# Performance work log

Measured on AMD Instinct MI355X. Metric: run time of the kernel, lower is better.

The kernel has to match this reference:

```python
import jax, jax.numpy as jnp
import numpy as np

NUM_HEADS = 16

def _rms_norm(x):
    # F.rms_norm over last dim, eps = dtype machine epsilon (torch default eps=None)
    eps = jnp.finfo(jnp.float32).eps
    ms = jnp.mean(jnp.square(x.astype(jnp.float32)), axis=-1, keepdims=True)
    return (x.astype(jnp.float32) * jax.lax.rsqrt(ms + eps)).astype(x.dtype)

def _rotary_tables(T, head_dim):
    # inv_freq = (1/1024)**linspace(0,1,head_dim//4), padded with zeros to head_dim//2
    quarter = head_dim // 4
    inv_freq = (1.0 / 1024.0) ** jnp.linspace(0.0, 1.0, quarter, dtype=jnp.float32)
    inv_freq = jnp.concatenate([inv_freq, jnp.zeros(quarter, dtype=jnp.float32)])
    t = jnp.arange(T, dtype=jnp.float32)
    theta = t[:, None] * inv_freq[None, :]          # [T, head_dim//2]
    return jnp.cos(theta), jnp.sin(theta)

def _rotary(x, cos, sin):
    # x: [B, T, H, hd]; rotate in fp32, cast back
    xf = x.astype(jnp.float32)
    x1, x2 = jnp.split(xf, 2, axis=-1)
    c = cos[None, :, None, :]
    s = sin[None, :, None, :]
    y1 = x1 * c + x2 * s
    y2 = -x1 * s + x2 * c
    return jnp.concatenate([y1, y2], axis=-1).astype(x.dtype)

def setup_inputs() -> dict:
    key = jax.random.key(0)
    ks = jax.random.split(key, 7)
    B, T, D = 1, 2048, 1024
    sc = 1.0 / np.sqrt(D)
    return {
        "x": jax.random.normal(ks[0], (B, T, D), jnp.float32),
        "vi": jax.random.normal(ks[1], (B, T, D), jnp.float32),
        "Wq": jax.random.normal(ks[2], (D, D), jnp.float32) * sc,
        "Wk": jax.random.normal(ks[3], (D, D), jnp.float32) * sc,
        "Wv": jax.random.normal(ks[4], (D, D), jnp.float32) * sc,
        "Wproj": jax.random.normal(ks[5], (D, D), jnp.float32) * sc,
        "lambdas": jnp.array([0.5, 0.5], jnp.float32),
    }

def reference(x, vi, Wq, Wk, Wv, Wproj, lambdas):
    B, T, D = x.shape
    H = NUM_HEADS
    hd = D // H
    q = (x @ Wq.T).reshape(B, T, H, hd)
    k = (x @ Wk.T).reshape(B, T, H, hd)
    v = (x @ Wv.T).reshape(B, T, H, hd)
    # value residual: lambda-mixed v
    v = lambdas[0] * v + lambdas[1] * vi.reshape(B, T, H, hd)
    q, k = _rms_norm(q), _rms_norm(k)
    cos, sin = _rotary_tables(T, hd)
    q, k = _rotary(q, cos, sin), _rotary(k, cos, sin)
    # causal attention, default flex_attention scale = 1/sqrt(head_dim)
    scores = jnp.einsum('bthd,bshd->bhts', q, k) / jnp.sqrt(jnp.float32(hd))
    causal = jnp.tril(jnp.ones((T, T), dtype=bool))
    scores = jnp.where(causal[None, None], scores, jnp.float32(-1e30))
    attn = jax.nn.softmax(scores, axis=-1)
    y = jnp.einsum('bhts,bshd->bthd', attn, v).reshape(B, T, D)
    return y @ Wproj.T
```

## Files before the change

### kernel.cpp

```cpp
#include <hip/hip_runtime.h>
#include <math.h>

#define T_SEQ 2048
#define D_MODEL 1024
#define NH 16
#define HD 64

typedef unsigned short ushort_t;
typedef unsigned int uint_t;
typedef short short8 __attribute__((ext_vector_type(8)));
typedef float floatx4 __attribute__((ext_vector_type(4)));

__device__ __forceinline__ ushort_t f2bf(float f) {
    uint_t u = __float_as_uint(f);
    u += 0x7FFFu + ((u >> 16) & 1u);
    return (ushort_t)(u >> 16);
}
__device__ __forceinline__ uint_t pack2(float a, float b) {
    return (uint_t)f2bf(a) | ((uint_t)f2bf(b) << 16);
}
__device__ __forceinline__ void cp16(ushort_t* dst, const ushort_t* src) {
    uint4 a = ((const uint4*)src)[0];
    uint4 b = ((const uint4*)src)[1];
    ((uint4*)dst)[0] = a;
    ((uint4*)dst)[1] = b;
}
__device__ __forceinline__ void gload16(const ushort_t* g, ushort_t* l) {
    __builtin_amdgcn_global_load_lds(
        (const __attribute__((address_space(1))) void*)g,
        (__attribute__((address_space(3))) void*)l, 16, 0, 0);
}

#define LDK 72

__global__ __launch_bounds__(256) void to_bf16(
        const float* __restrict__ x,  const float* __restrict__ wq,
        const float* __restrict__ wk, const float* __restrict__ wv,
        const float* __restrict__ wp,
        ushort_t* __restrict__ xb,  ushort_t* __restrict__ wqb,
        ushort_t* __restrict__ wkb, ushort_t* __restrict__ wvb,
        ushort_t* __restrict__ wpb)
{
    size_t i = (size_t)blockIdx.x * 256 + threadIdx.x;
    const float* src; ushort_t* dst; size_t off;
    if (i < 262144)      { src = x;  dst = xb;  off = i; }
    else if (i < 393216) { src = wq; dst = wqb; off = i - 262144; }
    else if (i < 524288) { src = wk; dst = wkb; off = i - 393216; }
    else if (i < 655360) { src = wv; dst = wvb; off = i - 524288; }
    else                 { src = wp; dst = wpb; off = i - 655360; }
    float4 f0 = ((const float4*)src)[off * 2];
    float4 f1 = ((const float4*)src)[off * 2 + 1];
    uint4 u;
    u.x = pack2(f0.x, f0.y); u.y = pack2(f0.z, f0.w);
    u.z = pack2(f1.x, f1.y); u.w = pack2(f1.z, f1.w);
    ((uint4*)dst)[off] = u;
}

__global__ __launch_bounds__(256) void gemm_qkv(
        const ushort_t* __restrict__ xb,
        const ushort_t* __restrict__ Wqb, const ushort_t* __restrict__ Wkb,
        const ushort_t* __restrict__ Wvb,
        const float* __restrict__ vi, const float* __restrict__ lam,
        ushort_t* __restrict__ qb, ushort_t* __restrict__ kb,
        ushort_t* __restrict__ vbt)
{
    const int z = blockIdx.z;
    const ushort_t* __restrict__ W = (z == 0) ? Wqb : (z == 1) ? Wkb : Wvb;
    const int row0 = blockIdx.y * 64;
    const int col0 = blockIdx.x * 128;

    __shared__ ushort_t As[2 * 64 * 64];
    __shared__ ushort_t Bs[2 * 128 * 64];

    const int tid = threadIdx.x;
    const int wave = tid >> 6, lane = tid & 63;
    const int wm = wave >> 1, wn = wave & 1;
    const int l15 = lane & 15, quad = lane >> 4;
    const int srow  = tid >> 3;
    const int sslot = (tid & 7) ^ (srow & 7);

    floatx4 acc[2][4];
    #pragma unroll
    for (int i = 0; i < 2; ++i)
        #pragma unroll
        for (int j = 0; j < 4; ++j)
            acc[i][j] = (floatx4){0.f, 0.f, 0.f, 0.f};

    auto stageAB = [&](int k0, int p) {
        ushort_t* Ap = As + p * 4096;
        ushort_t* Bp = Bs + p * 8192;
        #pragma unroll
        for (int c = 0; c < 2; ++c)
            gload16(xb + (size_t)(row0 + c * 32 + srow) * D_MODEL + k0 + sslot * 8,
                    Ap + c * 2048 + tid * 8);
        #pragma unroll
        for (int c = 0; c < 4; ++c)
            gload16(W + (size_t)(col0 + c * 32 + srow) * D_MODEL + k0 + sslot * 8,
                    Bp + c * 2048 + tid * 8);
    };

    stageAB(0, 0);
    int cur = 0;
    for (int knext = 64; knext <= D_MODEL; knext += 64) {
        const bool haveNext = (knext < D_MODEL);
        if (haveNext) {
            stageAB(knext, cur ^ 1);
            asm volatile("s_waitcnt vmcnt(6)" ::: "memory");
        } else {
            asm volatile("s_waitcnt vmcnt(0)" ::: "memory");
        }
        __builtin_amdgcn_s_barrier();
        const ushort_t* Ac = As + cur * 4096;
        const ushort_t* Bc = Bs + cur * 8192;
        #pragma unroll
        for (int kh = 0; kh < 2; ++kh) {
            const int slot = ((kh * 4 + quad) ^ (l15 & 7)) << 3;
            short8 a[2], b[4];
            #pragma unroll
            for (int i = 0; i < 2; ++i)
                a[i] = *(const short8*)(Ac + (32 * wm + i * 16 + l15) * 64 + slot);
            #pragma unroll
            for (int j = 0; j < 4; ++j)
                b[j] = *(const short8*)(Bc + (64 * wn + j * 16 + l15) * 64 + slot);
            #pragma unroll
            for (int i = 0; i < 2; ++i)
                #pragma unroll
                for (int j = 0; j < 4; ++j)
                    acc[i][j] = __builtin_amdgcn_mfma_f32_16x16x32_bf16(a[i], b[j], acc[i][j], 0, 0, 0);
        }
        asm volatile("" ::: "memory");
        __builtin_amdgcn_s_barrier();
        cur ^= 1;
    }

    if (z < 2) {
        ushort_t* __restrict__ o = (z == 0) ? qb : kb;
        const float oscale = (z == 0) ? 0.125f : 1.0f;
        const int hbase = col0 + 64 * wn;
        const float eps = 1.1920929e-7f;
        const float fr = exp2f(-10.0f * (float)l15 / 15.0f);
        #pragma unroll
        for (int i = 0; i < 2; ++i)
            #pragma unroll
            for (int r = 0; r < 4; ++r) {
                const int t = row0 + 32 * wm + i * 16 + quad * 4 + r;
                float v0 = acc[i][0][r], v1 = acc[i][1][r];
                float v2 = acc[i][2][r], v3 = acc[i][3][r];
                float ss = v0 * v0 + v1 * v1 + v2 * v2 + v3 * v3;
                ss += __shfl_xor(ss, 1);
                ss += __shfl_xor(ss, 2);
                ss += __shfl_xor(ss, 4);
                ss += __shfl_xor(ss, 8);
                const float sc = rsqrtf(ss * (1.0f / 64.0f) + eps);
                v0 *= sc; v1 *= sc; v2 *= sc; v3 *= sc;
                const float th = (float)t * fr;
                const float cs = cosf(th), sn = sinf(th);
                const float y0 = v0 * cs + v2 * sn;
                const float y2 = v2 * cs - v0 * sn;
                const size_t rb = (size_t)t * D_MODEL + hbase;
                o[rb +  0 + l15] = f2bf(y0 * oscale);
                o[rb + 16 + l15] = f2bf(v1 * oscale);
                o[rb + 32 + l15] = f2bf(y2 * oscale);
                o[rb + 48 + l15] = f2bf(v3 * oscale);
            }
    } else {
        const float l0 = lam[0], l1 = lam[1];
        #pragma unroll
        for (int i = 0; i < 2; ++i)
            #pragma unroll
            for (int j = 0; j < 4; ++j) {
                const int tb = row0 + 32 * wm + i * 16 + quad * 4;
                const int jj = col0 + 64 * wn + j * 16 + l15;
                float b0 = l0 * acc[i][j][0] + l1 * vi[(size_t)(tb + 0) * D_MODEL + jj];
                float b1 = l0 * acc[i][j][1] + l1 * vi[(size_t)(tb + 1) * D_MODEL + jj];
                float b2 = l0 * acc[i][j][2] + l1 * vi[(size_t)(tb + 2) * D_MODEL + jj];
                float b3 = l0 * acc[i][j][3] + l1 * vi[(size_t)(tb + 3) * D_MODEL + jj];
                uint2 u;
                u.x = pack2(b0, b1);
                u.y = pack2(b2, b3);
                *(uint2*)(vbt + (size_t)jj * T_SEQ + tb) = u;
            }
    }
}

__global__ __launch_bounds__(256) void attn(
        const ushort_t* __restrict__ qb, const ushort_t* __restrict__ kb,
        const ushort_t* __restrict__ vbt, ushort_t* __restrict__ yb,
        float* __restrict__ Opart, float* __restrict__ Lpart)
{
    const int h = blockIdx.y;
    const int x = blockIdx.x;
    int qt, ct_begin, ct_end, pidx;
    if (x < 16) {
        qt = 31 - x;
        const int mid = (qt + 2) >> 1;
        ct_begin = 0; ct_end = mid;
        pidx = ((h * 16 + (qt - 16)) << 1);
    } else if (x < 32) {
        qt = 47 - x;
        const int mid = (qt + 2) >> 1;
        ct_begin = mid; ct_end = qt + 1;
        pidx = ((h * 16 + (qt - 16)) << 1) + 1;
    } else {
        qt = 47 - x;
        ct_begin = 0; ct_end = qt + 1;
        pidx = -1;
    }
    const int t0 = qt * 64;

    __shared__ ushort_t Ks[2 * 64 * 64];
    __shared__ ushort_t Vs[2 * 64 * 64];
    __shared__ ushort_t QPs[64 * LDK];

    const int tid = threadIdx.x;
    const int wave = tid >> 6, lane = tid & 63;
    const int l15 = lane & 15, quad = lane >> 4;
    const int r4 = tid >> 2, c4 = (tid & 3) * 16;
    const int srow  = tid >> 3;
    const int sslot = (tid & 7) ^ (srow & 7);
    const int bx = l15 & 7;

    cp16(QPs + r4 * LDK + c4, qb + (size_t)(t0 + r4) * D_MODEL + h * HD + c4);
    __syncthreads();
    short8 qf[2];
    qf[0] = *(const short8*)(QPs + (16 * wave + l15) * LDK + 0  + quad * 8);
    qf[1] = *(const short8*)(QPs + (16 * wave + l15) * LDK + 32 + quad * 8);

    auto stageKV = [&](int kt, int p) {
        const int s0 = kt * 64;
        ushort_t* Kp = Ks + p * 4096;
        ushort_t* Vp = Vs + p * 4096;
        gload16(kb  + (size_t)(s0 + srow)      * D_MODEL + h * HD + sslot * 8, Kp + tid * 8);
        gload16(kb  + (size_t)(s0 + 32 + srow) * D_MODEL + h * HD + sslot * 8, Kp + 2048 + tid * 8);
        gload16(vbt + (size_t)(h * HD + srow)      * T_SEQ + s0 + sslot * 8,   Vp + tid * 8);
        gload16(vbt + (size_t)(h * HD + 32 + srow) * T_SEQ + s0 + sslot * 8,   Vp + 2048 + tid * 8);
    };

    float l_acc[4];
    floatx4 O[4];
    #pragma unroll
    for (int r = 0; r < 4; ++r) l_acc[r] = 0.0f;
    #pragma unroll
    for (int d = 0; d < 4; ++d) O[d] = (floatx4){0.f, 0.f, 0.f, 0.f};

    stageKV(ct_begin, 0);
    int cur = 0;
    for (int kt = ct_begin; kt < ct_end; ++kt) {
        const bool haveNext = (kt + 1 < ct_end);
        if (haveNext) {
            stageKV(kt + 1, cur ^ 1);
            asm volatile("s_waitcnt vmcnt(4)" ::: "memory");
        } else {
            asm volatile("s_waitcnt vmcnt(0)" ::: "memory");
        }
        __builtin_amdgcn_s_barrier();

        const ushort_t* Kc = Ks + cur * 4096;
        const ushort_t* Vc = Vs + cur * 4096;

        floatx4 sa[4];
        #pragma unroll
        for (int ct = 0; ct < 4; ++ct) {
            const ushort_t* krow = Kc + (ct * 16 + l15) * 64;
            short8 b0 = *(const short8*)(krow + ((quad ^ bx) << 3));
            short8 b1 = *(const short8*)(krow + (((quad + 4) ^ bx) << 3));
            floatx4 t4 = (floatx4){0.f, 0.f, 0.f, 0.f};
            t4 = __builtin_amdgcn_mfma_f32_16x16x32_bf16(qf[0], b0, t4, 0, 0, 0);
            t4 = __builtin_amdgcn_mfma_f32_16x16x32_bf16(qf[1], b1, t4, 0, 0, 0);
            sa[ct] = t4;
        }
        if (kt == qt) {
            #pragma unroll
            for (int ct = 0; ct < 4; ++ct)
                #pragma unroll
                for (int r = 0; r < 4; ++r) {
                    int trow = 16 * wave + quad * 4 + r;
                    int scol = ct * 16 + l15;
                    if (scol > trow) sa[ct][r] = -1e30f;
                }
        }
        float p[4][4];
        #pragma unroll
        for (int ct = 0; ct < 4; ++ct)
            #pragma unroll
            for (int r = 0; r < 4; ++r) {
                p[ct][r] = __expf(sa[ct][r] - 8.0f);
                l_acc[r] += p[ct][r];
            }

        #pragma unroll
        for (int ct = 0; ct < 4; ++ct)
            #pragma unroll
            for (int r = 0; r < 4; ++r)
                QPs[(16 * wave + quad * 4 + r) * LDK + ct * 16 + l15] = f2bf(p[ct][r]);

        short8 pa0 = *(const short8*)(QPs + (16 * wave + l15) * LDK + 0  + quad * 8);
        short8 pa1 = *(const short8*)(QPs + (16 * wave + l15) * LDK + 32 + quad * 8);
        #pragma unroll
        for (int dt = 0; dt < 4; ++dt) {
            const ushort_t* vrow = Vc + (dt * 16 + l15) * 64;
            short8 vb0 = *(const short8*)(vrow + ((quad ^ bx) << 3));
            short8 vb1 = *(const short8*)(vrow + (((quad + 4) ^ bx) << 3));
            O[dt] = __builtin_amdgcn_mfma_f32_16x16x32_bf16(pa0, vb0, O[dt], 0, 0, 0);
            O[dt] = __builtin_amdgcn_mfma_f32_16x16x32_bf16(pa1, vb1, O[dt], 0, 0, 0);
        }

        asm volatile("" ::: "memory");
        __builtin_amdgcn_s_barrier();
        cur ^= 1;
    }

    float l_run[4];
    #pragma unroll
    for (int r = 0; r < 4; ++r) {
        float s = l_acc[r];
        s += __shfl_xor(s, 1);
        s += __shfl_xor(s, 2);
        s += __shfl_xor(s, 4);
        s += __shfl_xor(s, 8);
        l_run[r] = s;
    }

    if (pidx < 0) {
        #pragma unroll
        for (int r = 0; r < 4; ++r) {
            const float inv_l = 1.0f / l_run[r];
            const int t = t0 + 16 * wave + quad * 4 + r;
            #pragma unroll
            for (int dt = 0; dt < 4; ++dt)
                yb[(size_t)t * D_MODEL + h * HD + dt * 16 + l15] = f2bf(O[dt][r] * inv_l);
        }
    } else {
        float* __restrict__ Op = Opart + (size_t)pidx * 4096;
        #pragma unroll
        for (int r = 0; r < 4; ++r) {
            const int row = 16 * wave + quad * 4 + r;
            #pragma unroll
            for (int dt = 0; dt < 4; ++dt)
                Op[row * 64 + dt * 16 + l15] = O[dt][r];
            if (l15 == 0) Lpart[(size_t)pidx * 64 + row] = l_run[r];
        }
    }
}

__global__ __launch_bounds__(256) void attn_combine(
        const float* __restrict__ Opart, const float* __restrict__ Lpart,
        ushort_t* __restrict__ yb)
{
    const int qtp = blockIdx.x;
    const int h   = blockIdx.y;
    const int tid = threadIdx.x;
    const int row  = tid >> 2;
    const int dseg = (tid & 3) * 16;
    const int p0 = (h * 16 + qtp) * 2;

    const float l0 = Lpart[(size_t)p0 * 64 + row];
    const float l1 = Lpart[((size_t)p0 + 1) * 64 + row];
    const float inv = 1.0f / (l0 + l1);

    const float* O0 = Opart + (size_t)p0 * 4096 + row * 64 + dseg;
    const float* O1 = O0 + 4096;

    uint_t u[8];
    #pragma unroll
    for (int g = 0; g < 4; ++g) {
        float4 a = ((const float4*)O0)[g];
        float4 b = ((const float4*)O1)[g];
        u[g * 2 + 0] = pack2((a.x + b.x) * inv, (a.y + b.y) * inv);
        u[g * 2 + 1] = pack2((a.z + b.z) * inv, (a.w + b.w) * inv);
    }
    const int t = (16 + qtp) * 64 + row;
    uint4* dst = (uint4*)(yb + (size_t)t * D_MODEL + h * HD + dseg);
    dst[0] = make_uint4(u[0], u[1], u[2], u[3]);
    dst[1] = make_uint4(u[4], u[5], u[6], u[7]);
}

__global__ __launch_bounds__(256) void gemm_proj(
        const ushort_t* __restrict__ yb, const ushort_t* __restrict__ Wpb,
        float* __restrict__ out)
{
    const int row0 = blockIdx.y * 64;
    const int col0 = blockIdx.x * 128;

    __shared__ ushort_t As[2 * 64 * 64];
    __shared__ ushort_t Bs[2 * 128 * 64];

    const int tid = threadIdx.x;
    const int wave = tid >> 6, lane = tid & 63;
    const int wm = wave >> 1, wn = wave & 1;
    const int l15 = lane & 15, quad = lane >> 4;
    const int srow  = tid >> 3;
    const int sslot = (tid & 7) ^ (srow & 7);

    floatx4 acc[2][4];
    #pragma unroll
    for (int i = 0; i < 2; ++i)
        #pragma unroll
        for (int j = 0; j < 4; ++j)
            acc[i][j] = (floatx4){0.f, 0.f, 0.f, 0.f};

    auto stageAB = [&](int k0, int p) {
        ushort_t* Ap = As + p * 4096;
        ushort_t* Bp = Bs + p * 8192;
        #pragma unroll
        for (int c = 0; c < 2; ++c)
            gload16(yb + (size_t)(row0 + c * 32 + srow) * D_MODEL + k0 + sslot * 8,
                    Ap + c * 2048 + tid * 8);
        #pragma unroll
        for (int c = 0; c < 4; ++c)
            gload16(Wpb + (size_t)(col0 + c * 32 + srow) * D_MODEL + k0 + sslot * 8,
                    Bp + c * 2048 + tid * 8);
    };

    stageAB(0, 0);
    int cur = 0;
    for (int knext = 64; knext <= D_MODEL; knext += 64) {
        const bool haveNext = (knext < D_MODEL);
        if (haveNext) {
            stageAB(knext, cur ^ 1);
            asm volatile("s_waitcnt vmcnt(6)" ::: "memory");
        } else {
            asm volatile("s_waitcnt vmcnt(0)" ::: "memory");
        }
        __builtin_amdgcn_s_barrier();
        const ushort_t* Ac = As + cur * 4096;
        const ushort_t* Bc = Bs + cur * 8192;
        #pragma unroll
        for (int kh = 0; kh < 2; ++kh) {
            const int slot = ((kh * 4 + quad) ^ (l15 & 7)) << 3;
            short8 a[2], b[4];
            #pragma unroll
            for (int i = 0; i < 2; ++i)
                a[i] = *(const short8*)(Ac + (32 * wm + i * 16 + l15) * 64 + slot);
            #pragma unroll
            for (int j = 0; j < 4; ++j)
                b[j] = *(const short8*)(Bc + (64 * wn + j * 16 + l15) * 64 + slot);
            #pragma unroll
            for (int i = 0; i < 2; ++i)
                #pragma unroll
                for (int j = 0; j < 4; ++j)
                    acc[i][j] = __builtin_amdgcn_mfma_f32_16x16x32_bf16(a[i], b[j], acc[i][j], 0, 0, 0);
        }
        asm volatile("" ::: "memory");
        __builtin_amdgcn_s_barrier();
        cur ^= 1;
    }

    #pragma unroll
    for (int i = 0; i < 2; ++i)
        #pragma unroll
        for (int j = 0; j < 4; ++j) {
            const int t = row0 + 32 * wm + i * 16 + quad * 4;
            const int jj = col0 + 64 * wn + j * 16 + l15;
            #pragma unroll
            for (int r = 0; r < 4; ++r)
                out[(size_t)(t + r) * D_MODEL + jj] = acc[i][j][r];
        }
}

extern "C" void kernel_launch(void* const* d_in, const int* in_sizes, int n_in,
                              void* d_out, int out_size, void* d_ws, size_t ws_size,
                              hipStream_t stream) {
    (void)in_sizes; (void)n_in; (void)out_size; (void)ws_size;
    const float* x   = (const float*)d_in[0];
    const float* vi  = (const float*)d_in[1];
    const float* Wq  = (const float*)d_in[2];
    const float* Wk  = (const float*)d_in[3];
    const float* Wv  = (const float*)d_in[4];
    const float* Wp  = (const float*)d_in[5];
    const float* lam = (const float*)d_in[6];

    char* base = (char*)d_ws;
    ushort_t* xb  = (ushort_t*)(base);
    ushort_t* wqb = (ushort_t*)(base + (size_t)4  * 1048576);
    ushort_t* wkb = (ushort_t*)(base + (size_t)6  * 1048576);
    ushort_t* wvb = (ushort_t*)(base + (size_t)8  * 1048576);
    ushort_t* wpb = (ushort_t*)(base + (size_t)10 * 1048576);
    ushort_t* qb  = (ushort_t*)(base + (size_t)12 * 1048576);
    ushort_t* kb  = (ushort_t*)(base + (size_t)16 * 1048576);
    ushort_t* vbt = (ushort_t*)(base + (size_t)20 * 1048576);
    ushort_t* yb  = (ushort_t*)(base + (size_t)24 * 1048576);
    float* Opart  = (float*)(base);
    float* Lpart  = (float*)(base + (size_t)8 * 1048576);
    float* out = (float*)d_out;

    to_bf16<<<dim3(786432 / 256), 256, 0, stream>>>(x, Wq, Wk, Wv, Wp, xb, wqb, wkb, wvb, wpb);
    gemm_qkv<<<dim3(8, 32, 3), 256, 0, stream>>>(xb, wqb, wkb, wvb, vi, lam, qb, kb, vbt);
    attn<<<dim3(48, 16), 256, 0, stream>>>(qb, kb, vbt, yb, Opart, Lpart);
    attn_combine<<<dim3(16, 16), 256, 0, stream>>>(Opart, Lpart, yb);
    gemm_proj<<<dim3(8, 32), 256, 0, stream>>>(yb, wpb, out);
}
```

Measured before the change: 149.7 us.

## Enlarge GEMM tiles to 128 rows and rebalance attention split-K across query tiles

Both projection GEMMs now use 128x128 output tiles per block with 4x4 MFMA accumulators per wave, which doubles A-tile reuse and halves the grid. The attention grid is reorganised with head as the fast dimension. The longest query tiles are split three ways and the middle ones two ways to balance causal work, and the combine kernel now sums a variable number of partials. Lpart moves into the output buffer before the final GEMM overwrites it. The changes add register and LDS pressure and reduce the number of blocks in the GEMMs.

Measured after the change: 154.4 us. 1.03x slower.

```diff
diff --git a/kernel.cpp b/kernel.cpp
--- a/kernel.cpp
+++ b/kernel.cpp
@@ -66,10 +66,10 @@
 {
     const int z = blockIdx.z;
     const ushort_t* __restrict__ W = (z == 0) ? Wqb : (z == 1) ? Wkb : Wvb;
-    const int row0 = blockIdx.y * 64;
+    const int row0 = blockIdx.y * 128;
     const int col0 = blockIdx.x * 128;
 
-    __shared__ ushort_t As[2 * 64 * 64];
+    __shared__ ushort_t As[2 * 128 * 64];
     __shared__ ushort_t Bs[2 * 128 * 64];
 
     const int tid = threadIdx.x;
@@ -79,18 +79,18 @@
     const int srow  = tid >> 3;
     const int sslot = (tid & 7) ^ (srow & 7);
 
-    floatx4 acc[2][4];
-    #pragma unroll
-    for (int i = 0; i < 2; ++i)
+    floatx4 acc[4][4];
+    #pragma unroll
+    for (int i = 0; i < 4; ++i)
         #pragma unroll
         for (int j = 0; j < 4; ++j)
             acc[i][j] = (floatx4){0.f, 0.f, 0.f, 0.f};
 
     auto stageAB = [&](int k0, int p) {
-        ushort_t* Ap = As + p * 4096;
+        ushort_t* Ap = As + p * 8192;
         ushort_t* Bp = Bs + p * 8192;
         #pragma unroll
-        for (int c = 0; c < 2; ++c)
+        for (int c = 0; c < 4; ++c)
             gload16(xb + (size_t)(row0 + c * 32 + srow) * D_MODEL + k0 + sslot * 8,
                     Ap + c * 2048 + tid * 8);
         #pragma unroll
@@ -105,25 +105,25 @@
         const bool haveNext = (knext < D_MODEL);
         if (haveNext) {
             stageAB(knext, cur ^ 1);
-            asm volatile("s_waitcnt vmcnt(6)" ::: "memory");
+            asm volatile("s_waitcnt vmcnt(8)" ::: "memory");
         } else {
             asm volatile("s_waitcnt vmcnt(0)" ::: "memory");
         }
         __builtin_amdgcn_s_barrier();
-        const ushort_t* Ac = As + cur * 4096;
+        const ushort_t* Ac = As + cur * 8192;
         const ushort_t* Bc = Bs + cur * 8192;
         #pragma unroll
         for (int kh = 0; kh < 2; ++kh) {
             const int slot = ((kh * 4 + quad) ^ (l15 & 7)) << 3;
-            short8 a[2], b[4];
-            #pragma unroll
-            for (int i = 0; i < 2; ++i)
-                a[i] = *(const short8*)(Ac + (32 * wm + i * 16 + l15) * 64 + slot);
+            short8 a[4], b[4];
+            #pragma unroll
+            for (int i = 0; i < 4; ++i)
+                a[i] = *(const short8*)(Ac + (64 * wm + i * 16 + l15) * 64 + slot);
             #pragma unroll
             for (int j = 0; j < 4; ++j)
                 b[j] = *(const short8*)(Bc + (64 * wn + j * 16 + l15) * 64 + slot);
             #pragma unroll
-            for (int i = 0; i < 2; ++i)
+            for (int i = 0; i < 4; ++i)
                 #pragma unroll
                 for (int j = 0; j < 4; ++j)
                     acc[i][j] = __builtin_amdgcn_mfma_f32_16x16x32_bf16(a[i], b[j], acc[i][j], 0, 0, 0);
@@ -140,10 +140,10 @@
         const float eps = 1.1920929e-7f;
         const float fr = exp2f(-10.0f * (float)l15 / 15.0f);
         #pragma unroll
-        for (int i = 0; i < 2; ++i)
+        for (int i = 0; i < 4; ++i)
             #pragma unroll
             for (int r = 0; r < 4; ++r) {
-                const int t = row0 + 32 * wm + i * 16 + quad * 4 + r;
+                const int t = row0 + 64 * wm + i * 16 + quad * 4 + r;
                 float v0 = acc[i][0][r], v1 = acc[i][1][r];
                 float v2 = acc[i][2][r], v3 = acc[i][3][r];
                 float ss = v0 * v0 + v1 * v1 + v2 * v2 + v3 * v3;
@@ -166,10 +166,10 @@
     } else {
         const float l0 = lam[0], l1 = lam[1];
         #pragma unroll
-        for (int i = 0; i < 2; ++i)
+        for (int i = 0; i < 4; ++i)
             #pragma unroll
             for (int j = 0; j < 4; ++j) {
-                const int tb = row0 + 32 * wm + i * 16 + quad * 4;
+                const int tb = row0 + 64 * wm + i * 16 + quad * 4;
                 const int jj = col0 + 64 * wn + j * 16 + l15;
                 float b0 = l0 * acc[i][j][0] + l1 * vi[(size_t)(tb + 0) * D_MODEL + jj];
                 float b1 = l0 * acc[i][j][1] + l1 * vi[(size_t)(tb + 1) * D_MODEL + jj];
@@ -188,21 +188,28 @@
         const ushort_t* __restrict__ vbt, ushort_t* __restrict__ yb,
         float* __restrict__ Opart, float* __restrict__ Lpart)
 {
-    const int h = blockIdx.y;
-    const int x = blockIdx.x;
+    const int h = blockIdx.x;
+    const int x = blockIdx.y;
     int qt, ct_begin, ct_end, pidx;
-    if (x < 16) {
-        qt = 31 - x;
-        const int mid = (qt + 2) >> 1;
-        ct_begin = 0; ct_end = mid;
-        pidx = ((h * 16 + (qt - 16)) << 1);
-    } else if (x < 32) {
-        qt = 47 - x;
-        const int mid = (qt + 2) >> 1;
-        ct_begin = mid; ct_end = qt + 1;
-        pidx = ((h * 16 + (qt - 16)) << 1) + 1;
+    if (x < 28) {
+        qt = 27 - (x >> 1);
+        const int w = qt + 1;
+        const int c0 = (w + 1) >> 1;
+        if ((x & 1) == 0) { ct_begin = 0;  ct_end = c0; }
+        else              { ct_begin = c0; ct_end = w;  }
+        pidx = h * 40 + 12 + (qt - 14) * 2 + (x & 1);
+    } else if (x < 40) {
+        const int xx = x - 28;
+        qt = 28 + xx / 3;
+        const int c = xx % 3;
+        const int w = qt + 1;
+        const int b0 = (w + 2) / 3;
+        const int b1 = (2 * w + 2) / 3;
+        ct_begin = (c == 0) ? 0  : (c == 1) ? b0 : b1;
+        ct_end   = (c == 0) ? b0 : (c == 1) ? b1 : w;
+        pidx = h * 40 + (qt - 28) * 3 + c;
     } else {
-        qt = 47 - x;
+        qt = 53 - x;
         ct_begin = 0; ct_end = qt + 1;
         pidx = -1;
     }
@@ -347,29 +354,41 @@
         const float* __restrict__ Opart, const float* __restrict__ Lpart,
         ushort_t* __restrict__ yb)
 {
-    const int qtp = blockIdx.x;
-    const int h   = blockIdx.y;
+    const int h  = blockIdx.x;
+    const int qt = 14 + (int)blockIdx.y;
     const int tid = threadIdx.x;
     const int row  = tid >> 2;
     const int dseg = (tid & 3) * 16;
-    const int p0 = (h * 16 + qtp) * 2;
-
-    const float l0 = Lpart[(size_t)p0 * 64 + row];
-    const float l1 = Lpart[((size_t)p0 + 1) * 64 + row];
-    const float inv = 1.0f / (l0 + l1);
-
-    const float* O0 = Opart + (size_t)p0 * 4096 + row * 64 + dseg;
-    const float* O1 = O0 + 4096;
+    int s0, nc;
+    if (qt >= 28) { s0 = (qt - 28) * 3;        nc = 3; }
+    else          { s0 = 12 + (qt - 14) * 2;   nc = 2; }
+    const int p0 = h * 40 + s0;
+
+    float accv[16];
+    #pragma unroll
+    for (int e = 0; e < 16; ++e) accv[e] = 0.0f;
+    float lsum = 0.0f;
+    for (int c = 0; c < nc; ++c) {
+        const float* Op = Opart + (size_t)(p0 + c) * 4096 + row * 64 + dseg;
+        lsum += Lpart[(size_t)(p0 + c) * 64 + row];
+        #pragma unroll
+        for (int g = 0; g < 4; ++g) {
+            float4 a = ((const float4*)Op)[g];
+            accv[g * 4 + 0] += a.x;
+            accv[g * 4 + 1] += a.y;
+            accv[g * 4 + 2] += a.z;
+            accv[g * 4 + 3] += a.w;
+        }
+    }
+    const float inv = 1.0f / lsum;
 
     uint_t u[8];
     #pragma unroll
     for (int g = 0; g < 4; ++g) {
-        float4 a = ((const float4*)O0)[g];
-        float4 b = ((const float4*)O1)[g];
-        u[g * 2 + 0] = pack2((a.x + b.x) * inv, (a.y + b.y) * inv);
-        u[g * 2 + 1] = pack2((a.z + b.z) * inv, (a.w + b.w) * inv);
-    }
-    const int t = (16 + qtp) * 64 + row;
+        u[g * 2 + 0] = pack2(accv[g * 4 + 0] * inv, accv[g * 4 + 1] * inv);
+        u[g * 2 + 1] = pack2(accv[g * 4 + 2] * inv, accv[g * 4 + 3] * inv);
+    }
+    const int t = qt * 64 + row;
     uint4* dst = (uint4*)(yb + (size_t)t * D_MODEL + h * HD + dseg);
     dst[0] = make_uint4(u[0], u[1], u[2], u[3]);
     dst[1] = make_uint4(u[4], u[5], u[6], u[7]);
@@ -379,10 +398,10 @@
         const ushort_t* __restrict__ yb, const ushort_t* __restrict__ Wpb,
         float* __restrict__ out)
 {
-    const int row0 = blockIdx.y * 64;
+    const int row0 = blockIdx.y * 128;
     const int col0 = blockIdx.x * 128;
 
-    __shared__ ushort_t As[2 * 64 * 64];
+    __shared__ ushort_t As[2 * 128 * 64];
     __shared__ ushort_t Bs[2 * 128 * 64];
 
     const int tid = threadIdx.x;
@@ -392,18 +411,18 @@
     const int srow  = tid >> 3;
     const int sslot = (tid & 7) ^ (srow & 7);
 
-    floatx4 acc[2][4];
-    #pragma unroll
-    for (int i = 0; i < 2; ++i)
+    floatx4 acc[4][4];
+    #pragma unroll
+    for (int i = 0; i < 4; ++i)
         #pragma unroll
         for (int j = 0; j < 4; ++j)
             acc[i][j] = (floatx4){0.f, 0.f, 0.f, 0.f};
 
     auto stageAB = [&](int k0, int p) {
-        ushort_t* Ap = As + p * 4096;
+        ushort_t* Ap = As + p * 8192;
         ushort_t* Bp = Bs + p * 8192;
         #pragma unroll
-        for (int c = 0; c < 2; ++c)
+        for (int c = 0; c < 4; ++c)
             gload16(yb + (size_t)(row0 + c * 32 + srow) * D_MODEL + k0 + sslot * 8,
                     Ap + c * 2048 + tid * 8);
         #pragma unroll
@@ -418,25 +437,25 @@
         const bool haveNext = (knext < D_MODEL);
         if (haveNext) {
             stageAB(knext, cur ^ 1);
-            asm volatile("s_waitcnt vmcnt(6)" ::: "memory");
+            asm volatile("s_waitcnt vmcnt(8)" ::: "memory");
         } else {
             asm volatile("s_waitcnt vmcnt(0)" ::: "memory");
         }
         __builtin_amdgcn_s_barrier();
-        const ushort_t* Ac = As + cur * 4096;
+        const ushort_t* Ac = As + cur * 8192;
         const ushort_t* Bc = Bs + cur * 8192;
         #pragma unroll
         for (int kh = 0; kh < 2; ++kh) {
             const int slot = ((kh * 4 + quad) ^ (l15 & 7)) << 3;
-            short8 a[2], b[4];
-            #pragma unroll
-            for (int i = 0; i < 2; ++i)
-                a[i] = *(const short8*)(Ac + (32 * wm + i * 16 + l15) * 64 + slot);
+            short8 a[4], b[4];
+            #pragma unroll
+            for (int i = 0; i < 4; ++i)
+                a[i] = *(const short8*)(Ac + (64 * wm + i * 16 + l15) * 64 + slot);
             #pragma unroll
             for (int j = 0; j < 4; ++j)
                 b[j] = *(const short8*)(Bc + (64 * wn + j * 16 + l15) * 64 + slot);
             #pragma unroll
-            for (int i = 0; i < 2; ++i)
+            for (int i = 0; i < 4; ++i)
                 #pragma unroll
                 for (int j = 0; j < 4; ++j)
                     acc[i][j] = __builtin_amdgcn_mfma_f32_16x16x32_bf16(a[i], b[j], acc[i][j], 0, 0, 0);
@@ -447,10 +466,10 @@
     }
 
     #pragma unroll
-    for (int i = 0; i < 2; ++i)
+    for (int i = 0; i < 4; ++i)
         #pragma unroll
         for (int j = 0; j < 4; ++j) {
-            const int t = row0 + 32 * wm + i * 16 + quad * 4;
+            const int t = row0 + 64 * wm + i * 16 + quad * 4;
             const int jj = col0 + 64 * wn + j * 16 + l15;
             #pragma unroll
             for (int r = 0; r < 4; ++r)
@@ -481,12 +500,12 @@
     ushort_t* vbt = (ushort_t*)(base + (size_t)20 * 1048576);
     ushort_t* yb  = (ushort_t*)(base + (size_t)24 * 1048576);
     float* Opart  = (float*)(base);
-    float* Lpart  = (float*)(base + (size_t)8 * 1048576);
+    float* Lpart  = (float*)d_out;
     float* out = (float*)d_out;
 
     to_bf16<<<dim3(786432 / 256), 256, 0, stream>>>(x, Wq, Wk, Wv, Wp, xb, wqb, wkb, wvb, wpb);
-    gemm_qkv<<<dim3(8, 32, 3), 256, 0, stream>>>(xb, wqb, wkb, wvb, vi, lam, qb, kb, vbt);
-    attn<<<dim3(48, 16), 256, 0, stream>>>(qb, kb, vbt, yb, Opart, Lpart);
-    attn_combine<<<dim3(16, 16), 256, 0, stream>>>(Opart, Lpart, yb);
-    gemm_proj<<<dim3(8, 32), 256, 0, stream>>>(yb, wpb, out);
-}
+    gemm_qkv<<<dim3(8, 16, 3), 256, 0, stream>>>(xb, wqb, wkb, wvb, vi, lam, qb, kb, vbt);
+    attn<<<dim3(16, 54), 256, 0, stream>>>(qb, kb, vbt, yb, Opart, Lpart);
+    attn_combine<<<dim3(16, 18), 256, 0, stream>>>(Opart, Lpart, yb);
+    gemm_proj<<<dim3(8, 16), 256, 0, stream>>>(yb, wpb, out);
+}
```
